# Kernel tuning notes

Hardware: AMD Instinct MI355X
Metric: run time of the kernel (lower is better)

## Reference

```python
import jax, jax.numpy as jnp
import numpy as np
import math

IN_DIM = 256
OUT_DIM = 256
MAX_IN = 1024
MAX_OUT = 512
BATCH = 2
SEQ = 1024  # actual_seq_len == max_in_seq here
RED = 2
LN_EPS = 1e-5


def setup_inputs() -> dict:
    key = jax.random.key(0)
    ks = jax.random.split(key, 8)
    N = BATCH * SEQ
    return {
        "x": jax.random.normal(ks[0], (N, IN_DIM), dtype=jnp.float32),
        "M": jax.random.uniform(ks[1], (OUT_DIM, IN_DIM), minval=-0.5, maxval=0.5, dtype=jnp.float32),
        "P": jax.random.uniform(ks[2], (OUT_DIM, OUT_DIM), minval=-0.1, maxval=0.1, dtype=jnp.float32),
        "Linker": jax.random.uniform(ks[3], (MAX_IN, MAX_OUT), minval=-0.1, maxval=0.1, dtype=jnp.float32),
        "ln_gamma": jnp.ones((OUT_DIM,), dtype=jnp.float32),
        "ln_beta": jnp.zeros((OUT_DIM,), dtype=jnp.float32),
        "res_W": jax.random.uniform(ks[4], (OUT_DIM, IN_DIM), minval=-0.1, maxval=0.1, dtype=jnp.float32),
        "res_linker": jax.random.uniform(ks[5], (MAX_IN, MAX_OUT), minval=-0.1, maxval=0.1, dtype=jnp.float32),
        "actual_seq_len": SEQ,
    }


def _layer_norm(z, gamma, beta):
    mu = jnp.mean(z, axis=-1, keepdims=True)
    var = jnp.mean((z - mu) ** 2, axis=-1, keepdims=True)
    return (z - mu) * jax.lax.rsqrt(var + LN_EPS) * gamma + beta


def _periods():
    i = jnp.arange(OUT_DIM, dtype=jnp.float32)[:, None]
    j = jnp.arange(OUT_DIM, dtype=jnp.float32)[None, :]
    return i * OUT_DIM + j + 2.0  # (D, D)


def reference(x, M, P, Linker, ln_gamma, ln_beta, res_W, res_linker, actual_seq_len):
    S = int(actual_seq_len)
    N, _ = x.shape
    B = N // S
    D = OUT_DIM
    out_seq = max(1, S // RED)

    # Z = LN(x @ M^T)
    Z = _layer_norm(x @ M.T, ln_gamma, ln_beta)  # (N, D)

    # position transform: T[k,i] = sum_j Z[k,j] * P[i,j] * cos(2*pi*k / periods[i,j])
    k = jnp.arange(N, dtype=jnp.float32)[:, None, None]  # (N,1,1)
    phi = jnp.cos(2.0 * math.pi * k / _periods()[None])   # (N, D, D)
    T = jnp.einsum('kj,ij,kij->ki', Z, P, phi)            # (N, D)

    # adaptive sequence-length transform via Linker slice
    L = Linker[:S, :out_seq]                               # (S, out_seq)
    U = jnp.einsum('bsd,st->btd', T.reshape(B, S, D), L).reshape(B * out_seq, D)

    # 'separate' residual path
    rfeat = (x @ res_W.T).reshape(B, S, D)
    rL = res_linker[:S, :out_seq]
    residual = jnp.einsum('bsd,st->btd', rfeat, rL).reshape(B * out_seq, D)

    return U + residual
```

## Files before the change

kernel.cpp:

```cpp
#include <hip/hip_runtime.h>

#define D256 256
#define KT 8
#define S_SEQ 1024
#define OUTSEQ 512

typedef __attribute__((ext_vector_type(8))) short bf16x8;
typedef __attribute__((ext_vector_type(8))) unsigned short u16x8;
typedef __attribute__((ext_vector_type(4))) float f32x4;

__device__ inline unsigned short f2bf(float f) {
  unsigned u = __float_as_uint(f);
  return (unsigned short)((u + 0x7fffu + ((u >> 16) & 1u)) >> 16);
}

__global__ __launch_bounds__(256) void k_prep(const float* __restrict__ x,
                                              const float* __restrict__ M,
                                              const float* __restrict__ resW,
                                              const float* __restrict__ P,
                                              const float* __restrict__ Linker,
                                              const float* __restrict__ rLinker,
                                              float4* __restrict__ PIt4,
                                              unsigned short* __restrict__ LinkTb,
                                              unsigned short* __restrict__ xb,
                                              unsigned short* __restrict__ Mb,
                                              unsigned short* __restrict__ Wb) {
  __shared__ float tl[64][65];
  const int tid = threadIdx.x;
  const int blk = blockIdx.x;
  if (blk < 256) {
    const int j = blk;
    const int t = tid;
    const float p = (float)(t * D256 + j + 2);
    const float ip = 1.0f / p;
    const float cb2 = 2.0f * __builtin_amdgcn_cosf(ip);
    PIt4[j * D256 + t] = make_float4(P[t * D256 + j], ip, cb2, 0.0f);
    return;
  }
  if (blk >= 512) {
    const float* src;
    unsigned short* dst;
    size_t base;
    if (blk < 768)      { src = x;    dst = xb; base = (size_t)(blk - 512) * 2048; }
    else if (blk < 800) { src = M;    dst = Mb; base = (size_t)(blk - 768) * 2048; }
    else                { src = resW; dst = Wb; base = (size_t)(blk - 800) * 2048; }
    const size_t off = base + (size_t)tid * 8;
    const float4 v0 = *(const float4*)(src + off);
    const float4 v1 = *(const float4*)(src + off + 4);
    u16x8 o;
    o[0] = f2bf(v0.x); o[1] = f2bf(v0.y); o[2] = f2bf(v0.z); o[3] = f2bf(v0.w);
    o[4] = f2bf(v1.x); o[5] = f2bf(v1.y); o[6] = f2bf(v1.z); o[7] = f2bf(v1.w);
    *(u16x8*)(dst + off) = o;
    return;
  }
  const int tb = blk - 256;
  const int st = tb & 31;
  const int tt = tb >> 5;
  const int s0 = st * 64, t0 = tt * 64;
  const float* src = (s0 < 1024) ? (Linker + (size_t)s0 * OUTSEQ)
                                 : (rLinker + (size_t)(s0 - 1024) * OUTSEQ);
  {
    const int sy = tid >> 2, sx = tid & 3;
    #pragma unroll
    for (int c = 0; c < 4; ++c) {
      const int ci = sx + c * 4;
      const float4 v = *(const float4*)&src[sy * OUTSEQ + t0 + ci * 4];
      tl[ci * 4 + 0][sy] = v.x;
      tl[ci * 4 + 1][sy] = v.y;
      tl[ci * 4 + 2][sy] = v.z;
      tl[ci * 4 + 3][sy] = v.w;
    }
  }
  __syncthreads();
  {
    const int ty = tid >> 2, tx = tid & 3;
    u16x8 o0, o1;
    #pragma unroll
    for (int e = 0; e < 8; ++e) o0[e] = f2bf(tl[ty][tx * 16 + e]);
    #pragma unroll
    for (int e = 0; e < 8; ++e) o1[e] = f2bf(tl[ty][tx * 16 + 8 + e]);
    unsigned short* dst = LinkTb + (size_t)(t0 + ty) * 2048 + s0 + tx * 16;
    *(u16x8*)dst = o0;
    *(u16x8*)(dst + 8) = o1;
  }
}

__global__ __launch_bounds__(256) void k_Azn(const unsigned short* __restrict__ xb,
                                             const unsigned short* __restrict__ Mb,
                                             const unsigned short* __restrict__ Wb,
                                             const float* __restrict__ gamma,
                                             const float* __restrict__ beta,
                                             float* __restrict__ Zb,
                                             unsigned short* __restrict__ Bt) {
  __shared__ float Zs[16][D256];
  __shared__ float Rs[16][D256];
  __shared__ float mu_s[16], rs_s[16];
  const int k0 = blockIdx.x * 16;
  const int w = threadIdx.x >> 6;
  const int l = threadIdx.x & 63;
  const int m = l & 15, q = l >> 4;

  f32x4 aZ[4] = {}, aR[4] = {};
  const unsigned short* Arow = xb + (size_t)(k0 + m) * D256;
  #pragma unroll
  for (int ks = 0; ks < 8; ++ks) {
    const bf16x8 a = *(const bf16x8*)(Arow + ks * 32 + q * 8);
    #pragma unroll
    for (int cf = 0; cf < 4; ++cf) {
      const int o = w * 64 + cf * 16 + m;
      const bf16x8 bz = *(const bf16x8*)(Mb + (size_t)o * D256 + ks * 32 + q * 8);
      const bf16x8 br = *(const bf16x8*)(Wb + (size_t)o * D256 + ks * 32 + q * 8);
      aZ[cf] = __builtin_amdgcn_mfma_f32_16x16x32_bf16(a, bz, aZ[cf], 0, 0, 0);
      aR[cf] = __builtin_amdgcn_mfma_f32_16x16x32_bf16(a, br, aR[cf], 0, 0, 0);
    }
  }
  #pragma unroll
  for (int cf = 0; cf < 4; ++cf) {
    #pragma unroll
    for (int r = 0; r < 4; ++r) {
      Zs[q * 4 + r][w * 64 + cf * 16 + m] = aZ[cf][r];
      Rs[q * 4 + r][w * 64 + cf * 16 + m] = aR[cf][r];
    }
  }
  __syncthreads();

  #pragma unroll
  for (int rr = w; rr < 16; rr += 4) {
    float s = 0.f, sq = 0.f;
    #pragma unroll
    for (int p = 0; p < 4; ++p) {
      const float v = Zs[rr][l + 64 * p];
      s += v;
      sq = fmaf(v, v, sq);
    }
    #pragma unroll
    for (int off = 32; off; off >>= 1) {
      s += __shfl_down(s, off);
      sq += __shfl_down(sq, off);
    }
    if (l == 0) {
      const float mu = s * (1.0f / 256.0f);
      const float var = sq * (1.0f / 256.0f) - mu * mu;
      mu_s[rr] = mu;
      rs_s[rr] = rsqrtf(var + 1e-5f);
    }
  }
  __syncthreads();

  {
    const int t = threadIdx.x;
    const float g = gamma[t], be = beta[t];
    u16x8 o0, o1;
    #pragma unroll
    for (int rr = 0; rr < 16; ++rr) {
      Zb[(size_t)(k0 + rr) * D256 + t] = (Zs[rr][t] - mu_s[rr]) * rs_s[rr] * g + be;
      const unsigned short rb = f2bf(Rs[rr][t]);
      if (rr < 8) o0[rr] = rb; else o1[rr - 8] = rb;
    }
    unsigned short* dst = Bt + (size_t)t * 4096 + 2048 + k0;
    *(u16x8*)dst = o0;
    *(u16x8*)(dst + 8) = o1;
  }
}

__global__ __launch_bounds__(512) void k_B(const float* __restrict__ Zb,
                                           const float4* __restrict__ PIt4,
                                           unsigned short* __restrict__ Bt) {
  __shared__ float Xs[D256][12];
  __shared__ float red[4][KT][128];
  const int tid = threadIdx.x;
  const int il = tid & 127;
  const int jq = tid >> 7;
  const int kt = blockIdx.x >> 1;
  const int ih = blockIdx.x & 1;
  const int k0 = kt * KT;
  const int ib = ih * 128 + il;

  {
    const int i = tid & 255;
    const int h2 = tid >> 8;
    #pragma unroll
    for (int r = 0; r < 4; ++r)
      Xs[i][h2 * 4 + r] = Zb[(size_t)(k0 + h2 * 4 + r) * D256 + i];
  }
  __syncthreads();

  float accT[KT] = {};
  const float kf0 = (float)k0, kf1 = (float)(k0 + 1);
  {
    const float4* pip = PIt4 + ib;
    #pragma unroll 4
    for (int jj = 0; jj < 64; ++jj) {
      const int j = jq * 64 + jj;
      const float4 pi = pip[(size_t)j * D256];
      const float4 z0 = *(const float4*)&Xs[j][0];
      const float4 z1 = *(const float4*)&Xs[j][4];
      const float r0 = __builtin_amdgcn_fractf(kf0 * pi.y);
      const float r1 = __builtin_amdgcn_fractf(kf1 * pi.y);
      float c0 = __builtin_amdgcn_cosf(r0);
      float c1 = __builtin_amdgcn_cosf(r1);
      accT[0] = fmaf(z0.x * pi.x, c0, accT[0]);
      accT[1] = fmaf(z0.y * pi.x, c1, accT[1]);
      float c2;
      c2 = fmaf(pi.z, c1, -c0); accT[2] = fmaf(z0.z * pi.x, c2, accT[2]); c0 = c1; c1 = c2;
      c2 = fmaf(pi.z, c1, -c0); accT[3] = fmaf(z0.w * pi.x, c2, accT[3]); c0 = c1; c1 = c2;
      c2 = fmaf(pi.z, c1, -c0); accT[4] = fmaf(z1.x * pi.x, c2, accT[4]); c0 = c1; c1 = c2;
      c2 = fmaf(pi.z, c1, -c0); accT[5] = fmaf(z1.y * pi.x, c2, accT[5]); c0 = c1; c1 = c2;
      c2 = fmaf(pi.z, c1, -c0); accT[6] = fmaf(z1.z * pi.x, c2, accT[6]); c0 = c1; c1 = c2;
      c2 = fmaf(pi.z, c1, -c0); accT[7] = fmaf(z1.w * pi.x, c2, accT[7]);
    }
  }
  #pragma unroll
  for (int r = 0; r < KT; ++r) red[jq][r][il] = accT[r];
  __syncthreads();
  if (tid < 128) {
    u16x8 o;
    #pragma unroll
    for (int r = 0; r < KT; ++r)
      o[r] = f2bf(red[0][r][tid] + red[1][r][tid] + red[2][r][tid] + red[3][r][tid]);
    *(u16x8*)(Bt + (size_t)(ih * 128 + tid) * 4096 + k0) = o;
  }
}

__global__ __launch_bounds__(256) void k_Cm(const unsigned short* __restrict__ LinkTb,
                                            const unsigned short* __restrict__ Bt,
                                            float* __restrict__ part) {
  const int bid = blockIdx.x;
  const int kc = bid & 7;
  const int dt = (bid >> 3) & 3;
  const int tt = (bid >> 5) & 7;
  const int b  = bid >> 8;
  const int wv = threadIdx.x >> 6;
  const int l  = threadIdx.x & 63;
  const int wm = wv >> 1, wn = wv & 1;
  const int t0 = tt * 64 + wm * 32;
  const int d0 = dt * 64 + wn * 32;
  const int m  = l & 15;
  const int q  = l >> 4;
  const int sc0 = kc * 128;

  f32x4 acc00 = {}, acc01 = {}, acc10 = {}, acc11 = {};
  const unsigned short* Arow = LinkTb + (size_t)(t0 + m) * 2048;
  const unsigned short* Brow = Bt + (size_t)(d0 + m) * 4096;

  #pragma unroll
  for (int seg = 0; seg < 2; ++seg) {
    const int acol = seg * 1024 + sc0 + q * 8;
    const int bcol = seg * 2048 + b * 1024 + sc0 + q * 8;
    #pragma unroll
    for (int ks = 0; ks < 4; ++ks) {
      const bf16x8 a0 = *(const bf16x8*)(Arow + acol + ks * 32);
      const bf16x8 a1 = *(const bf16x8*)(Arow + 16 * 2048 + acol + ks * 32);
      const bf16x8 b0 = *(const bf16x8*)(Brow + bcol + ks * 32);
      const bf16x8 b1 = *(const bf16x8*)(Brow + 16 * 4096 + bcol + ks * 32);
      acc00 = __builtin_amdgcn_mfma_f32_16x16x32_bf16(a0, b0, acc00, 0, 0, 0);
      acc01 = __builtin_amdgcn_mfma_f32_16x16x32_bf16(a0, b1, acc01, 0, 0, 0);
      acc10 = __builtin_amdgcn_mfma_f32_16x16x32_bf16(a1, b0, acc10, 0, 0, 0);
      acc11 = __builtin_amdgcn_mfma_f32_16x16x32_bf16(a1, b1, acc11, 0, 0, 0);
    }
  }

  float* pb = part + ((size_t)kc << 18) + (size_t)(b * 512 + t0 + q * 4) * D256 + d0 + m;
  #pragma unroll
  for (int reg = 0; reg < 4; ++reg) {
    pb[(0 + reg) * D256 + 0]   = acc00[reg];
    pb[(0 + reg) * D256 + 16]  = acc01[reg];
    pb[(16 + reg) * D256 + 0]  = acc10[reg];
    pb[(16 + reg) * D256 + 16] = acc11[reg];
  }
}

__global__ __launch_bounds__(256) void k_Cred(const float* __restrict__ part,
                                              float* __restrict__ out) {
  const int row = blockIdx.x;
  const int d   = threadIdx.x;
  float s = 0.f;
  #pragma unroll
  for (int kc = 0; kc < 8; ++kc)
    s += part[((size_t)kc << 18) + row * D256 + d];
  out[row * D256 + d] = s;
}

extern "C" void kernel_launch(void* const* d_in, const int* in_sizes, int n_in,
                              void* d_out, int out_size, void* d_ws, size_t ws_size,
                              hipStream_t stream) {
  const float* x       = (const float*)d_in[0];
  const float* M       = (const float*)d_in[1];
  const float* P       = (const float*)d_in[2];
  const float* Linker  = (const float*)d_in[3];
  const float* gamma   = (const float*)d_in[4];
  const float* beta    = (const float*)d_in[5];
  const float* resW    = (const float*)d_in[6];
  const float* rLinker = (const float*)d_in[7];
  float* out = (float*)d_out;

  char* ws = (char*)d_ws;
  float4*         PIt4   = (float4*)(ws);
  unsigned short* LinkTb = (unsigned short*)(ws + 1024 * 1024);
  unsigned short* Bt     = (unsigned short*)(ws + 3072 * 1024);
  unsigned short* xb     = (unsigned short*)(ws + 5120 * 1024);
  unsigned short* Mb     = (unsigned short*)(ws + 6144 * 1024);
  unsigned short* Wb     = (unsigned short*)(ws + 6272 * 1024);
  float*          Zb     = (float*)(ws + 6400 * 1024);
  float*          part   = (float*)(ws + 8448 * 1024);

  hipLaunchKernelGGL(k_prep, dim3(832),  dim3(256), 0, stream,
                     x, M, resW, P, Linker, rLinker, PIt4, LinkTb, xb, Mb, Wb);
  hipLaunchKernelGGL(k_Azn,  dim3(128),  dim3(256), 0, stream,
                     xb, Mb, Wb, gamma, beta, Zb, Bt);
  hipLaunchKernelGGL(k_B,    dim3(512),  dim3(512), 0, stream, Zb, PIt4, Bt);
  hipLaunchKernelGGL(k_Cm,   dim3(512),  dim3(256), 0, stream, LinkTb, Bt, part);
  hipLaunchKernelGGL(k_Cred, dim3(1024), dim3(256), 0, stream, part, out);
}
```

Baseline: 52.86 us.

## Retile position-transform kernel to 16 k rows per block with wide j split

Reworks the k_B cosine-weighted reduction. Each block now covers 16 sequence positions and 8 output features, with the j dimension split 32 ways across 256 threads, giving 4096 blocks instead of 512 blocks of 512 threads. The cosine recurrence is extended to 16 steps, which halves the hardware cos evaluations and the PIt4 traffic per output. The P weight is also folded into the seed cosines. The cost is a two-stage shared-memory reduction and a longer Chebyshev recurrence, which lets rounding error build up further.

```diff
diff --git a/kernel.cpp b/kernel.cpp
--- a/kernel.cpp
+++ b/kernel.cpp
@@ -7,6 +7,7 @@
 
 typedef __attribute__((ext_vector_type(8))) short bf16x8;
 typedef __attribute__((ext_vector_type(8))) unsigned short u16x8;
+typedef __attribute__((ext_vector_type(4))) unsigned short u16x4;
 typedef __attribute__((ext_vector_type(4))) float f32x4;
 
 __device__ inline unsigned short f2bf(float f) {
@@ -163,62 +164,78 @@
   }
 }
 
-__global__ __launch_bounds__(512) void k_B(const float* __restrict__ Zb,
-                                           const float4* __restrict__ PIt4,
-                                           unsigned short* __restrict__ Bt) {
-  __shared__ float Xs[D256][12];
-  __shared__ float red[4][KT][128];
+__global__ __launch_bounds__(256, 6) void k_B(const float* __restrict__ Zb,
+                                              const float4* __restrict__ PIt4,
+                                              unsigned short* __restrict__ Bt) {
+  __shared__ float buf[5120];
   const int tid = threadIdx.x;
-  const int il = tid & 127;
-  const int jq = tid >> 7;
-  const int kt = blockIdx.x >> 1;
-  const int ih = blockIdx.x & 1;
-  const int k0 = kt * KT;
-  const int ib = ih * 128 + il;
-
-  {
-    const int i = tid & 255;
-    const int h2 = tid >> 8;
-    #pragma unroll
-    for (int r = 0; r < 4; ++r)
-      Xs[i][h2 * 4 + r] = Zb[(size_t)(k0 + h2 * 4 + r) * D256 + i];
-  }
-  __syncthreads();
-
-  float accT[KT] = {};
-  const float kf0 = (float)k0, kf1 = (float)(k0 + 1);
-  {
-    const float4* pip = PIt4 + ib;
-    #pragma unroll 4
-    for (int jj = 0; jj < 64; ++jj) {
-      const int j = jq * 64 + jj;
-      const float4 pi = pip[(size_t)j * D256];
-      const float4 z0 = *(const float4*)&Xs[j][0];
-      const float4 z1 = *(const float4*)&Xs[j][4];
-      const float r0 = __builtin_amdgcn_fractf(kf0 * pi.y);
-      const float r1 = __builtin_amdgcn_fractf(kf1 * pi.y);
-      float c0 = __builtin_amdgcn_cosf(r0);
-      float c1 = __builtin_amdgcn_cosf(r1);
-      accT[0] = fmaf(z0.x * pi.x, c0, accT[0]);
-      accT[1] = fmaf(z0.y * pi.x, c1, accT[1]);
-      float c2;
-      c2 = fmaf(pi.z, c1, -c0); accT[2] = fmaf(z0.z * pi.x, c2, accT[2]); c0 = c1; c1 = c2;
-      c2 = fmaf(pi.z, c1, -c0); accT[3] = fmaf(z0.w * pi.x, c2, accT[3]); c0 = c1; c1 = c2;
-      c2 = fmaf(pi.z, c1, -c0); accT[4] = fmaf(z1.x * pi.x, c2, accT[4]); c0 = c1; c1 = c2;
-      c2 = fmaf(pi.z, c1, -c0); accT[5] = fmaf(z1.y * pi.x, c2, accT[5]); c0 = c1; c1 = c2;
-      c2 = fmaf(pi.z, c1, -c0); accT[6] = fmaf(z1.z * pi.x, c2, accT[6]); c0 = c1; c1 = c2;
-      c2 = fmaf(pi.z, c1, -c0); accT[7] = fmaf(z1.w * pi.x, c2, accT[7]);
-    }
-  }
-  #pragma unroll
-  for (int r = 0; r < KT; ++r) red[jq][r][il] = accT[r];
-  __syncthreads();
+  const int il = tid & 7;
+  const int jg = tid >> 3;
+  const int ig = blockIdx.x & 31;
+  const int kt = blockIdx.x >> 5;
+  const int i0 = ig * 8;
+  const int k0 = kt * 16;
+  const int i  = i0 + il;
+
+  #pragma unroll
+  for (int r = 0; r < 16; ++r)
+    buf[tid * 20 + r] = Zb[(size_t)(k0 + r) * D256 + tid];
+  __syncthreads();
+
+  float acc[16] = {};
+  const float kf0 = (float)k0;
+  const float4* pip = PIt4 + i;
+  #pragma unroll
+  for (int jj = 0; jj < 8; ++jj) {
+    const int j = jg + 32 * jj;
+    const float4 pi = pip[(size_t)j * D256];
+    const float4 z0 = *(const float4*)&buf[j * 20 + 0];
+    const float4 z1 = *(const float4*)&buf[j * 20 + 4];
+    const float4 z2 = *(const float4*)&buf[j * 20 + 8];
+    const float4 z3 = *(const float4*)&buf[j * 20 + 12];
+    const float a = kf0 * pi.y;
+    float c0 = __builtin_amdgcn_cosf(__builtin_amdgcn_fractf(a)) * pi.x;
+    float c1 = __builtin_amdgcn_cosf(__builtin_amdgcn_fractf(a + pi.y)) * pi.x;
+    acc[0] = fmaf(z0.x, c0, acc[0]);
+    acc[1] = fmaf(z0.y, c1, acc[1]);
+    float c2;
+    c2 = fmaf(pi.z, c1, -c0); acc[2]  = fmaf(z0.z, c2, acc[2]);  c0 = c1; c1 = c2;
+    c2 = fmaf(pi.z, c1, -c0); acc[3]  = fmaf(z0.w, c2, acc[3]);  c0 = c1; c1 = c2;
+    c2 = fmaf(pi.z, c1, -c0); acc[4]  = fmaf(z1.x, c2, acc[4]);  c0 = c1; c1 = c2;
+    c2 = fmaf(pi.z, c1, -c0); acc[5]  = fmaf(z1.y, c2, acc[5]);  c0 = c1; c1 = c2;
+    c2 = fmaf(pi.z, c1, -c0); acc[6]  = fmaf(z1.z, c2, acc[6]);  c0 = c1; c1 = c2;
+    c2 = fmaf(pi.z, c1, -c0); acc[7]  = fmaf(z1.w, c2, acc[7]);  c0 = c1; c1 = c2;
+    c2 = fmaf(pi.z, c1, -c0); acc[8]  = fmaf(z2.x, c2, acc[8]);  c0 = c1; c1 = c2;
+    c2 = fmaf(pi.z, c1, -c0); acc[9]  = fmaf(z2.y, c2, acc[9]);  c0 = c1; c1 = c2;
+    c2 = fmaf(pi.z, c1, -c0); acc[10] = fmaf(z2.z, c2, acc[10]); c0 = c1; c1 = c2;
+    c2 = fmaf(pi.z, c1, -c0); acc[11] = fmaf(z2.w, c2, acc[11]); c0 = c1; c1 = c2;
+    c2 = fmaf(pi.z, c1, -c0); acc[12] = fmaf(z3.x, c2, acc[12]); c0 = c1; c1 = c2;
+    c2 = fmaf(pi.z, c1, -c0); acc[13] = fmaf(z3.y, c2, acc[13]); c0 = c1; c1 = c2;
+    c2 = fmaf(pi.z, c1, -c0); acc[14] = fmaf(z3.z, c2, acc[14]); c0 = c1; c1 = c2;
+    c2 = fmaf(pi.z, c1, -c0); acc[15] = fmaf(z3.w, c2, acc[15]);
+  }
+  __syncthreads();
+
+  #pragma unroll
+  for (int k = 0; k < 16; ++k)
+    buf[jg * 132 + k * 8 + il] = acc[k];
+  __syncthreads();
+
+  float tv = 0.f;
   if (tid < 128) {
-    u16x8 o;
-    #pragma unroll
-    for (int r = 0; r < KT; ++r)
-      o[r] = f2bf(red[0][r][tid] + red[1][r][tid] + red[2][r][tid] + red[3][r][tid]);
-    *(u16x8*)(Bt + (size_t)(ih * 128 + tid) * 4096 + k0) = o;
+    #pragma unroll
+    for (int g = 0; g < 32; ++g) tv += buf[g * 132 + tid];
+  }
+  __syncthreads();
+  if (tid < 128) buf[(tid & 7) * 16 + (tid >> 3)] = tv;
+  __syncthreads();
+  if (tid < 32) {
+    const int iw = tid >> 2;
+    const int kq = tid & 3;
+    const float4 v = *(const float4*)&buf[iw * 16 + kq * 4];
+    u16x4 o;
+    o[0] = f2bf(v.x); o[1] = f2bf(v.y); o[2] = f2bf(v.z); o[3] = f2bf(v.w);
+    *(u16x4*)(Bt + (size_t)(i0 + iw) * 4096 + k0 + kq * 4) = o;
   }
 }
 
@@ -308,7 +325,7 @@
                      x, M, resW, P, Linker, rLinker, PIt4, LinkTb, xb, Mb, Wb);
   hipLaunchKernelGGL(k_Azn,  dim3(128),  dim3(256), 0, stream,
                      xb, Mb, Wb, gamma, beta, Zb, Bt);
-  hipLaunchKernelGGL(k_B,    dim3(512),  dim3(512), 0, stream, Zb, PIt4, Bt);
+  hipLaunchKernelGGL(k_B,    dim3(4096), dim3(256), 0, stream, Zb, PIt4, Bt);
   hipLaunchKernelGGL(k_Cm,   dim3(512),  dim3(256), 0, stream, LinkTb, Bt, part);
   hipLaunchKernelGGL(k_Cred, dim3(1024), dim3(256), 0, stream, part, out);
 }
```

Result: faster. 49.77 us (-5.9%).
